# Optimization experiments

Measured on AMD Instinct MI355X. Metric: run time of the kernel, lower is better.

Reference implementation:

```python
import jax, jax.numpy as jnp
import numpy as np

HEADS = 4
DIM_HEAD = 32
DIM = 128
HIDDEN = HEADS * DIM_HEAD  # 128


def setup_inputs() -> dict:
    key = jax.random.key(0)
    k1, k2, k3, k4 = jax.random.split(key, 4)
    B, C, H, W = 8, DIM, 128, 128
    x = jax.random.normal(k1, (B, C, H, W), dtype=jnp.float32)
    # 1x1 conv weights stored as [out_ch, in_ch] (kernel dims squeezed)
    w_qkv = jax.random.normal(k2, (3 * HIDDEN, DIM), dtype=jnp.float32) * (1.0 / np.sqrt(DIM))
    w_out = jax.random.normal(k3, (DIM, HIDDEN), dtype=jnp.float32) * (1.0 / np.sqrt(HIDDEN))
    b_out = jax.random.normal(k4, (DIM,), dtype=jnp.float32) * 0.01
    return {"x": x, "w_qkv": w_qkv, "w_out": w_out, "b_out": b_out}


def reference(x, w_qkv, w_out, b_out):
    b, c, h, w = x.shape
    n = h * w
    # 1x1 conv == per-pixel matmul over channels
    qkv = jnp.einsum('bchw,oc->bohw', x, w_qkv)            # [b, 3*HIDDEN, h, w]
    # channel layout: (qkv, heads, dim_head)
    qkv = qkv.reshape(b, 3, HEADS, DIM_HEAD, n)            # [b, 3, H, d, n]
    q, k, v = qkv[:, 0], qkv[:, 1], qkv[:, 2]
    k = jax.nn.softmax(k, axis=-1)                         # softmax over spatial n
    context = jnp.einsum('bhdn,bhen->bhde', k, v)          # [b, H, d, d] (tiny)
    out = jnp.einsum('bhde,bhdn->bhen', context, q)        # [b, H, d, n]
    out = out.reshape(b, HIDDEN, h, w)
    y = jnp.einsum('bchw,oc->bohw', out, w_out) + b_out[None, :, None, None]
    return y
```

## Files before the change

### kernel.cpp

```cpp
#include <hip/hip_runtime.h>
#include <math.h>

#define C_ 128
#define N_ 16384

#define WS_Z    0
#define WS_CTX  1024
#define WS_BMAT 33792
#define WS_A    164864
#define WS_PCTX 295936
#define WS_PZ   (WS_PCTX + 1024*4096)
#define WS_END  (WS_PZ + 512*128)

typedef __attribute__((ext_vector_type(8))) short bf16x8;
typedef __attribute__((ext_vector_type(4))) float f32x4;
typedef __attribute__((ext_vector_type(4))) unsigned int u32x4;
typedef __attribute__((ext_vector_type(2))) unsigned int u32x2;

__device__ __forceinline__ unsigned int pkbf(float a, float b) {
  unsigned int r;
  asm("v_cvt_pk_bf16_f32 %0, %1, %2" : "=v"(r) : "v"(a), "v"(b));
  return r;
}

__device__ __forceinline__ bf16x8 make_frag(float4 u, float4 v) {
  u32x4 q = {pkbf(u.x, u.y), pkbf(u.z, u.w), pkbf(v.x, v.y), pkbf(v.z, v.w)};
  return *(bf16x8*)&q;
}

__device__ __forceinline__ bf16x8 lds_frag16(const unsigned short* p) {
  u32x4 q = *(const u32x4*)p;
  return *(bf16x8*)&q;
}

__device__ __forceinline__ void load4(const float* p, float* o) {
  float4 v = *(const float4*)p;
  o[0] = v.x; o[1] = v.y; o[2] = v.z; o[3] = v.w;
}

__device__ __forceinline__ void* xsa(void* base, int row, int col_bytes) {
  return (void*)((char*)base + row * 272 + (col_bytes ^ (((row >> 2) & 7) << 4)));
}

template<bool ATOMIC>
__global__ __launch_bounds__(512, 2) void k1_kv_ctx(const float* __restrict__ x,
                                                    const float* __restrict__ wqkv,
                                                    float* __restrict__ ws) {
  __shared__ __attribute__((aligned(16))) unsigned short xs[64][136];
  __shared__ __attribute__((aligned(16))) unsigned short ekv[2][128][72];
  const int tid  = threadIdx.x;
  const int wave = tid >> 6;
  const int l15  = tid & 15;
  const int l4   = (tid >> 4) & 3;
  const int b    = blockIdx.y;
  const int j    = blockIdx.x;
  const int h    = wave & 3;
  const int t    = wave >> 2;
  const int kvrow0 = h * 32 + t * 128;
  const float* xb = x + (size_t)b * ((size_t)C_ * N_);

  const int sn4 = tid & 15;
  const int scq = tid >> 4;

  bf16x8 wf[2][4];
  #pragma unroll
  for (int mi = 0; mi < 2; ++mi)
    #pragma unroll
    for (int ki = 0; ki < 4; ++ki) {
      const float* p = wqkv + (size_t)(128 + kvrow0 + mi * 16 + l15) * C_ + ki * 32 + l4 * 8;
      wf[mi][ki] = make_frag(*(const float4*)p, *(const float4*)(p + 4));
    }

  {
    float va[4][4];
    #pragma unroll
    for (int r = 0; r < 4; ++r)
      load4(xb + (size_t)(scq * 4 + r) * N_ + j * 256 + sn4 * 4, va[r]);
    #pragma unroll
    for (int i = 0; i < 4; ++i) {
      u32x2 w = {pkbf(va[0][i], va[1][i]), pkbf(va[2][i], va[3][i])};
      *(u32x2*)xsa(xs, sn4 * 4 + i, scq * 8) = w;
    }
  }
  __syncthreads();

  const f32x4 z4 = {0.f, 0.f, 0.f, 0.f};
  f32x4 ctxacc[2][2];
  #pragma unroll
  for (int i = 0; i < 2; ++i)
    #pragma unroll
    for (int jj = 0; jj < 2; ++jj) ctxacc[i][jj] = z4;
  float zacc[2] = {0.f, 0.f};

  for (int st = 0; st < 4; ++st) {
    float pf[4][4];
    if (st < 3) {
      const int nbn = j * 256 + (st + 1) * 64;
      #pragma unroll
      for (int r = 0; r < 4; ++r)
        load4(xb + (size_t)(scq * 4 + r) * N_ + nbn + sn4 * 4, pf[r]);
    }

    #pragma unroll
    for (int half = 0; half < 2; ++half) {
      f32x4 acc[2][2];
      #pragma unroll
      for (int a = 0; a < 2; ++a)
        #pragma unroll
        for (int m = 0; m < 2; ++m) acc[a][m] = z4;
      #pragma unroll
      for (int ki = 0; ki < 4; ++ki) {
        bf16x8 bfr[2];
        #pragma unroll
        for (int ni2 = 0; ni2 < 2; ++ni2)
          bfr[ni2] = lds_frag16((const unsigned short*)
              xsa(xs, half * 32 + ni2 * 16 + l15, ki * 64 + l4 * 16));
        #pragma unroll
        for (int ni2 = 0; ni2 < 2; ++ni2)
          #pragma unroll
          for (int mi = 0; mi < 2; ++mi)
            acc[ni2][mi] = __builtin_amdgcn_mfma_f32_16x16x32_bf16(
                bfr[ni2], wf[mi][ki], acc[ni2][mi], 0, 0, 0);
      }
      #pragma unroll
      for (int ni2 = 0; ni2 < 2; ++ni2)
        #pragma unroll
        for (int mi = 0; mi < 2; ++mi) {
          float e0, e1, e2, e3;
          if (t == 0) {
            e0 = __expf(acc[ni2][mi][0]); e1 = __expf(acc[ni2][mi][1]);
            e2 = __expf(acc[ni2][mi][2]); e3 = __expf(acc[ni2][mi][3]);
            zacc[mi] += (e0 + e1) + (e2 + e3);
          } else {
            e0 = acc[ni2][mi][0]; e1 = acc[ni2][mi][1];
            e2 = acc[ni2][mi][2]; e3 = acc[ni2][mi][3];
          }
          u32x2 w = {pkbf(e0, e1), pkbf(e2, e3)};
          *(u32x2*)&ekv[t][h * 32 + mi * 16 + l15][(half * 2 + ni2) * 16 + l4 * 4] = w;
        }
    }
    __syncthreads();

    {
      bf16x8 af2[2], bv2[2];
      #pragma unroll
      for (int m2 = 0; m2 < 2; ++m2)
        af2[m2] = lds_frag16(&ekv[0][h * 32 + m2 * 16 + l15][t * 32 + l4 * 8]);
      #pragma unroll
      for (int n2 = 0; n2 < 2; ++n2)
        bv2[n2] = lds_frag16(&ekv[1][h * 32 + n2 * 16 + l15][t * 32 + l4 * 8]);
      #pragma unroll
      for (int m2 = 0; m2 < 2; ++m2)
        #pragma unroll
        for (int n2 = 0; n2 < 2; ++n2)
          ctxacc[m2][n2] = __builtin_amdgcn_mfma_f32_16x16x32_bf16(
              af2[m2], bv2[n2], ctxacc[m2][n2], 0, 0, 0);
    }

    if (st < 3) {
      #pragma unroll
      for (int i = 0; i < 4; ++i) {
        u32x2 w = {pkbf(pf[0][i], pf[1][i]), pkbf(pf[2][i], pf[3][i])};
        *(u32x2*)xsa(xs, sn4 * 4 + i, scq * 8) = w;
      }
    }
    __syncthreads();
  }

  if (!ATOMIC) {
    float* ps = ws + WS_PCTX + (size_t)((b * 64 + j) * 2 + t) * 4096 + h * 1024;
    #pragma unroll
    for (int m2 = 0; m2 < 2; ++m2)
      #pragma unroll
      for (int n2 = 0; n2 < 2; ++n2)
        #pragma unroll
        for (int r = 0; r < 4; ++r)
          ps[(m2 * 16 + l4 * 4 + r) * 32 + n2 * 16 + l15] = ctxacc[m2][n2][r];
  } else {
    float* ctx = ws + WS_CTX + (size_t)(b * 4 + h) * 1024;
    #pragma unroll
    for (int m2 = 0; m2 < 2; ++m2)
      #pragma unroll
      for (int n2 = 0; n2 < 2; ++n2)
        #pragma unroll
        for (int r = 0; r < 4; ++r)
          atomicAdd(&ctx[(m2 * 16 + l4 * 4 + r) * 32 + n2 * 16 + l15],
                    ctxacc[m2][n2][r]);
  }
  if (t == 0) {
    #pragma unroll
    for (int mi = 0; mi < 2; ++mi) {
      float z = zacc[mi];
      z += __shfl_xor(z, 16);
      z += __shfl_xor(z, 32);
      if ((tid & 48) == 0) {
        int row = h * 32 + mi * 16 + l15;
        if (!ATOMIC)
          ws[WS_PZ + (size_t)(b * 64 + j) * 128 + row] = z;
        else
          atomicAdd(&ws[WS_Z + b * 128 + row], z);
      }
    }
  }
}

__global__ __launch_bounds__(256) void k1b(float* __restrict__ ws) {
  const int tid = threadIdx.x;
  const int eq = blockIdx.x;
  const int h  = blockIdx.y;
  const int b  = blockIdx.z;
  const int el = eq * 256 + tid;
  const float* p = ws + WS_PCTX + (size_t)(b * 128) * 4096 + h * 1024 + el;
  float s = 0.f;
  #pragma unroll 8
  for (int jj = 0; jj < 128; ++jj) s += p[(size_t)jj * 4096];
  ws[WS_CTX + (size_t)(b * 4 + h) * 1024 + el] = s;
  if (eq == 0 && tid < 32) {
    const float* pz = ws + WS_PZ + (size_t)(b * 64) * 128 + h * 32 + tid;
    float z = 0.f;
    #pragma unroll 8
    for (int jj = 0; jj < 64; ++jj) z += pz[(size_t)jj * 128];
    ws[WS_Z + b * 128 + h * 32 + tid] = z;
  }
}

__global__ __launch_bounds__(256) void k2(const float* __restrict__ w_qkv,
                                          const float* __restrict__ w_out,
                                          float* __restrict__ ws) {
  __shared__ float bs[128][132];
  __shared__ float wqs[32][128];
  __shared__ float wos[32][132];
  __shared__ float cn[32][33];
  const int tid = threadIdx.x;
  const int oq = blockIdx.x, b = blockIdx.y;

  for (int h = 0; h < 4; ++h) {
    if (h) __syncthreads();
    const float* Z   = ws + WS_Z + b * 128 + h * 32;
    const float* ctx = ws + WS_CTX + ((b * 4 + h) * 32) * 32;
    #pragma unroll
    for (int k = 0; k < 4; ++k) {
      int idx = tid + k * 256;
      int d = idx >> 5, e = idx & 31;
      cn[d][e] = ctx[d * 32 + e] / Z[d];
    }
    #pragma unroll
    for (int k = 0; k < 4; ++k) {
      int idx = tid + k * 256;
      int d = idx >> 5, f4 = idx & 31;
      *(float4*)&wqs[d][f4 * 4] = *(const float4*)(w_qkv + (h * 32 + d) * 128 + f4 * 4);
    }
    __syncthreads();
    const int e = tid >> 3, cs = (tid & 7) * 16;
    float s[16];
    #pragma unroll
    for (int jj = 0; jj < 16; ++jj) s[jj] = 0.f;
    for (int d = 0; d < 32; ++d) {
      float v = cn[d][e];
      #pragma unroll
      for (int jj = 0; jj < 16; ++jj) s[jj] = fmaf(v, wqs[d][cs + jj], s[jj]);
    }
    #pragma unroll
    for (int jj = 0; jj < 16; ++jj) bs[h * 32 + e][cs + jj] = s[jj];
  }

  __syncthreads();
  #pragma unroll
  for (int k = 0; k < 4; ++k) {
    int idx = tid + k * 256;
    int r = idx >> 5, f4 = idx & 31;
    *(float4*)&wos[r][f4 * 4] = *(const float4*)(w_out + (oq * 32 + r) * 128 + f4 * 4);
  }
  __syncthreads();
  const int ol = tid >> 3, cq = (tid & 7) * 16;
  float s[16];
  #pragma unroll
  for (int jj = 0; jj < 16; ++jj) s[jj] = 0.f;
  for (int eg = 0; eg < 128; ++eg) {
    float w = wos[ol][eg];
    #pragma unroll
    for (int jj = 0; jj < 16; ++jj) s[jj] = fmaf(w, bs[eg][cq + jj], s[jj]);
  }
  float* A = ws + WS_A + ((size_t)b * 128 + oq * 32 + ol) * 128;
  #pragma unroll
  for (int jj = 0; jj < 16; ++jj) A[cq + jj] = s[jj];
}

__global__ __launch_bounds__(256, 2) void k3(const float* __restrict__ x,
                                             const float* __restrict__ bout,
                                             const float* __restrict__ ws,
                                             float* __restrict__ y) {
  __shared__ __attribute__((aligned(16))) unsigned short xs2[2][64][136];
  const int tid  = threadIdx.x;
  const int wave = tid >> 6;
  const int l15  = tid & 15;
  const int l4   = (tid >> 4) & 3;
  const int b    = blockIdx.y;
  const int n0   = blockIdx.x * 128;
  const float* xb = x + (size_t)b * ((size_t)C_ * N_);
  const float* A  = ws + WS_A + (size_t)b * 128 * 128;

  bf16x8 af[2][4];
  #pragma unroll
  for (int mi = 0; mi < 2; ++mi)
    #pragma unroll
    for (int ki = 0; ki < 4; ++ki) {
      const float* p = A + (size_t)(wave * 32 + mi * 16 + l15) * 128 + ki * 32 + l4 * 8;
      af[mi][ki] = make_frag(*(const float4*)p, *(const float4*)(p + 4));
    }
  float bias[2];
  #pragma unroll
  for (int mi = 0; mi < 2; ++mi) bias[mi] = bout[wave * 32 + mi * 16 + l15];

  #pragma unroll
  for (int it = 0; it < 2; ++it) {
    int idx = tid + it * 256;
    int n4 = idx & 15, cq = idx >> 4;
    float va[4][4];
    #pragma unroll
    for (int r = 0; r < 4; ++r)
      load4(xb + (size_t)(cq * 4 + r) * N_ + n0 + n4 * 4, va[r]);
    #pragma unroll
    for (int i = 0; i < 4; ++i) {
      u32x2 w = {pkbf(va[0][i], va[1][i]), pkbf(va[2][i], va[3][i])};
      *(u32x2*)xsa(&xs2[0][0][0], n4 * 4 + i, cq * 8) = w;
    }
  }
  __syncthreads();

  const f32x4 z4 = {0.f, 0.f, 0.f, 0.f};
  float* yb = y + (size_t)b * ((size_t)128 * N_);

  #pragma unroll
  for (int st = 0; st < 2; ++st) {
    const int nb = n0 + st * 64;
    f32x4 acc[4][2];
    #pragma unroll
    for (int ni = 0; ni < 4; ++ni)
      #pragma unroll
      for (int mi = 0; mi < 2; ++mi) acc[ni][mi] = z4;
    #pragma unroll
    for (int ki = 0; ki < 4; ++ki) {
      bf16x8 bfr[4];
      #pragma unroll
      for (int ni = 0; ni < 4; ++ni)
        bfr[ni] = lds_frag16((const unsigned short*)
            xsa(&xs2[st][0][0], ni * 16 + l15, ki * 64 + l4 * 16));
      #pragma unroll
      for (int ni = 0; ni < 4; ++ni)
        #pragma unroll
        for (int mi = 0; mi < 2; ++mi)
          acc[ni][mi] = __builtin_amdgcn_mfma_f32_16x16x32_bf16(
              bfr[ni], af[mi][ki], acc[ni][mi], 0, 0, 0);
    }

    if (st == 0) {
      #pragma unroll
      for (int it = 0; it < 2; ++it) {
        int idx = tid + it * 256;
        int n4 = idx & 15, cq = idx >> 4;
        float va[4][4];
        #pragma unroll
        for (int r = 0; r < 4; ++r)
          load4(xb + (size_t)(cq * 4 + r) * N_ + n0 + 64 + n4 * 4, va[r]);
        #pragma unroll
        for (int i = 0; i < 4; ++i) {
          u32x2 w = {pkbf(va[0][i], va[1][i]), pkbf(va[2][i], va[3][i])};
          *(u32x2*)xsa(&xs2[1][0][0], n4 * 4 + i, cq * 8) = w;
        }
      }
    }

    #pragma unroll
    for (int ni = 0; ni < 4; ++ni)
      #pragma unroll
      for (int mi = 0; mi < 2; ++mi) {
        float4 o;
        o.x = acc[ni][mi][0] + bias[mi];
        o.y = acc[ni][mi][1] + bias[mi];
        o.z = acc[ni][mi][2] + bias[mi];
        o.w = acc[ni][mi][3] + bias[mi];
        *(float4*)(yb + (size_t)(wave * 32 + mi * 16 + l15) * N_ + nb + ni * 16 + l4 * 4) = o;
      }

    if (st == 0) __syncthreads();
  }
}

extern "C" void kernel_launch(void* const* d_in, const int* in_sizes, int n_in,
                              void* d_out, int out_size, void* d_ws, size_t ws_size,
                              hipStream_t stream) {
  const float* x     = (const float*)d_in[0];
  const float* w_qkv = (const float*)d_in[1];
  const float* w_out = (const float*)d_in[2];
  const float* b_out = (const float*)d_in[3];
  float* y  = (float*)d_out;
  float* ws = (float*)d_ws;

  const bool partial = ws_size >= (size_t)WS_END * sizeof(float);
  if (partial) {
    k1_kv_ctx<false><<<dim3(64, 8), 512, 0, stream>>>(x, w_qkv, ws);
    k1b<<<dim3(4, 4, 8), 256, 0, stream>>>(ws);
  } else {
    hipMemsetAsync(ws, 0, (1024 + 32768) * sizeof(float), stream);
    k1_kv_ctx<true><<<dim3(64, 8), 512, 0, stream>>>(x, w_qkv, ws);
  }
  k2<<<dim3(4, 8), 256, 0, stream>>>(w_qkv, w_out, ws);
  k3<<<dim3(128, 8), 256, 0, stream>>>(x, b_out, ws, y);
}
```

Baseline: 84.40 us.

## Fuse partial-context reduction into per-head B-matrix kernel and split out projection

Merges the cross-block context/Z reduction into a new per-(head,batch) kernel that also normalizes the context and multiplies by the query weights, writing an intermediate B matrix to workspace. A separate kernel then loads B and applies the output projection, so the redundant per-oq recomputation of B across four heads in the old kernel goes away. The reduction now uses float4 loads but runs on only 32 blocks instead of 128. The LDS swizzle pattern in the x tile addressing is also changed.

New measurement: 77.77 us. -7.9%, faster.

```diff
diff --git a/kernel.cpp b/kernel.cpp
--- a/kernel.cpp
+++ b/kernel.cpp
@@ -39,7 +39,7 @@
 }
 
 __device__ __forceinline__ void* xsa(void* base, int row, int col_bytes) {
-  return (void*)((char*)base + row * 272 + (col_bytes ^ (((row >> 2) & 7) << 4)));
+  return (void*)((char*)base + row * 272 + (col_bytes ^ (((row >> 4) & 3) << 4)));
 }
 
 template<bool ATOMIC>
@@ -204,38 +204,39 @@
   }
 }
 
-__global__ __launch_bounds__(256) void k1b(float* __restrict__ ws) {
+template<bool PARTIAL>
+__global__ __launch_bounds__(256) void k2a(const float* __restrict__ w_qkv,
+                                           float* __restrict__ ws) {
+  __shared__ float cn[32][33];
+  __shared__ float wqs[32][128];
+  __shared__ float zsh[32];
   const int tid = threadIdx.x;
-  const int eq = blockIdx.x;
-  const int h  = blockIdx.y;
-  const int b  = blockIdx.z;
-  const int el = eq * 256 + tid;
-  const float* p = ws + WS_PCTX + (size_t)(b * 128) * 4096 + h * 1024 + el;
-  float s = 0.f;
-  #pragma unroll 8
-  for (int jj = 0; jj < 128; ++jj) s += p[(size_t)jj * 4096];
-  ws[WS_CTX + (size_t)(b * 4 + h) * 1024 + el] = s;
-  if (eq == 0 && tid < 32) {
-    const float* pz = ws + WS_PZ + (size_t)(b * 64) * 128 + h * 32 + tid;
-    float z = 0.f;
-    #pragma unroll 8
-    for (int jj = 0; jj < 64; ++jj) z += pz[(size_t)jj * 128];
-    ws[WS_Z + b * 128 + h * 32 + tid] = z;
-  }
-}
-
-__global__ __launch_bounds__(256) void k2(const float* __restrict__ w_qkv,
-                                          const float* __restrict__ w_out,
-                                          float* __restrict__ ws) {
-  __shared__ float bs[128][132];
-  __shared__ float wqs[32][128];
-  __shared__ float wos[32][132];
-  __shared__ float cn[32][33];
-  const int tid = threadIdx.x;
-  const int oq = blockIdx.x, b = blockIdx.y;
-
-  for (int h = 0; h < 4; ++h) {
-    if (h) __syncthreads();
+  const int h = blockIdx.x, b = blockIdx.y;
+
+  if (PARTIAL) {
+    const float* ps = ws + WS_PCTX + (size_t)(b * 128) * 4096 + h * 1024 + tid * 4;
+    float4 s = {0.f, 0.f, 0.f, 0.f};
+    #pragma unroll 4
+    for (int jj = 0; jj < 128; ++jj) {
+      float4 v = *(const float4*)(ps + (size_t)jj * 4096);
+      s.x += v.x; s.y += v.y; s.z += v.z; s.w += v.w;
+    }
+    if (tid < 32) {
+      const float* pz = ws + WS_PZ + (size_t)(b * 64) * 128 + h * 32 + tid;
+      float z = 0.f;
+      #pragma unroll 8
+      for (int jj = 0; jj < 64; ++jj) z += pz[(size_t)jj * 128];
+      zsh[tid] = z;
+    }
+    __syncthreads();
+    const int d = tid >> 3;
+    const int e0 = (tid * 4) & 31;
+    const float zz = zsh[d];
+    cn[d][e0 + 0] = s.x / zz;
+    cn[d][e0 + 1] = s.y / zz;
+    cn[d][e0 + 2] = s.z / zz;
+    cn[d][e0 + 3] = s.w / zz;
+  } else {
     const float* Z   = ws + WS_Z + b * 128 + h * 32;
     const float* ctx = ws + WS_CTX + ((b * 4 + h) * 32) * 32;
     #pragma unroll
@@ -244,34 +245,49 @@
       int d = idx >> 5, e = idx & 31;
       cn[d][e] = ctx[d * 32 + e] / Z[d];
     }
-    #pragma unroll
-    for (int k = 0; k < 4; ++k) {
-      int idx = tid + k * 256;
-      int d = idx >> 5, f4 = idx & 31;
-      *(float4*)&wqs[d][f4 * 4] = *(const float4*)(w_qkv + (h * 32 + d) * 128 + f4 * 4);
-    }
-    __syncthreads();
-    const int e = tid >> 3, cs = (tid & 7) * 16;
-    float s[16];
-    #pragma unroll
-    for (int jj = 0; jj < 16; ++jj) s[jj] = 0.f;
-    for (int d = 0; d < 32; ++d) {
-      float v = cn[d][e];
-      #pragma unroll
-      for (int jj = 0; jj < 16; ++jj) s[jj] = fmaf(v, wqs[d][cs + jj], s[jj]);
-    }
-    #pragma unroll
-    for (int jj = 0; jj < 16; ++jj) bs[h * 32 + e][cs + jj] = s[jj];
-  }
-
+  }
+  #pragma unroll
+  for (int k = 0; k < 4; ++k) {
+    int idx = tid + k * 256;
+    int d = idx >> 5, f4 = idx & 31;
+    *(float4*)&wqs[d][f4 * 4] = *(const float4*)(w_qkv + (h * 32 + d) * 128 + f4 * 4);
+  }
   __syncthreads();
-  #pragma unroll
+
+  const int e = tid >> 3, cs = (tid & 7) * 16;
+  float s[16];
+  #pragma unroll
+  for (int jj = 0; jj < 16; ++jj) s[jj] = 0.f;
+  for (int d = 0; d < 32; ++d) {
+    float v = cn[d][e];
+    #pragma unroll
+    for (int jj = 0; jj < 16; ++jj) s[jj] = fmaf(v, wqs[d][cs + jj], s[jj]);
+  }
+  float* Bm = ws + WS_BMAT + ((size_t)b * 128 + h * 32 + e) * 128;
+  #pragma unroll
+  for (int jj = 0; jj < 16; ++jj) Bm[cs + jj] = s[jj];
+}
+
+__global__ __launch_bounds__(256) void k2b(const float* __restrict__ w_out,
+                                           float* __restrict__ ws) {
+  __shared__ float bs[128][132];
+  __shared__ float wos[32][132];
+  const int tid = threadIdx.x;
+  const int oq = blockIdx.x, b = blockIdx.y;
+  const float* Bm = ws + WS_BMAT + (size_t)b * 128 * 128;
+
+  for (int k = 0; k < 16; ++k) {
+    int idx = tid + k * 256;
+    int r = idx >> 5, f4 = idx & 31;
+    *(float4*)&bs[r][f4 * 4] = *(const float4*)(Bm + r * 128 + f4 * 4);
+  }
   for (int k = 0; k < 4; ++k) {
     int idx = tid + k * 256;
     int r = idx >> 5, f4 = idx & 31;
     *(float4*)&wos[r][f4 * 4] = *(const float4*)(w_out + (oq * 32 + r) * 128 + f4 * 4);
   }
   __syncthreads();
+
   const int ol = tid >> 3, cq = (tid & 7) * 16;
   float s[16];
   #pragma unroll
@@ -400,11 +416,12 @@
   const bool partial = ws_size >= (size_t)WS_END * sizeof(float);
   if (partial) {
     k1_kv_ctx<false><<<dim3(64, 8), 512, 0, stream>>>(x, w_qkv, ws);
-    k1b<<<dim3(4, 4, 8), 256, 0, stream>>>(ws);
+    k2a<true><<<dim3(4, 8), 256, 0, stream>>>(w_qkv, ws);
   } else {
     hipMemsetAsync(ws, 0, (1024 + 32768) * sizeof(float), stream);
     k1_kv_ctx<true><<<dim3(64, 8), 512, 0, stream>>>(x, w_qkv, ws);
-  }
-  k2<<<dim3(4, 8), 256, 0, stream>>>(w_qkv, w_out, ws);
+    k2a<false><<<dim3(4, 8), 256, 0, stream>>>(w_qkv, ws);
+  }
+  k2b<<<dim3(4, 8), 256, 0, stream>>>(w_out, ws);
   k3<<<dim3(128, 8), 256, 0, stream>>>(x, b_out, ws, y);
 }
```
